# Kernel optimization log

Measured on AMD Instinct MI355X. Metric: run time of the kernel, lower is better.

## Reference

```python
import jax, jax.numpy as jnp
import numpy as np

B, S, D = 4, 1024, 1024
H, Dh = 16, 64
SPLATS_PER_LEVEL = [16, 32, 64]
LEVEL_W = [0.5, 0.3, 0.2]
TOPK = 64


def setup_inputs() -> dict:
    key = jax.random.key(0)
    ks = jax.random.split(key, 13)
    P = sum(SPLATS_PER_LEVEL)
    s = D ** -0.5
    inp = {
        'hidden_states': jax.random.normal(ks[0], (B, S, D), jnp.float32),
        'attention_mask': jnp.ones((B, S), jnp.float32),
        'Wq': jax.random.normal(ks[1], (D, H * Dh), jnp.float32) * s,
        'bq': jnp.zeros((H * Dh,), jnp.float32),
        'Wk': jax.random.normal(ks[2], (D, H * Dh), jnp.float32) * s,
        'bk': jnp.zeros((H * Dh,), jnp.float32),
        'Wv': jax.random.normal(ks[3], (D, H * Dh), jnp.float32) * s,
        'bv': jnp.zeros((H * Dh,), jnp.float32),
        'Wo': jax.random.normal(ks[4], (H * Dh, D), jnp.float32) * s,
        'bo': jnp.zeros((D,), jnp.float32),
    }
    # splat parameters in head_dim space (positions, full-covariance precisions, weights)
    mu = jax.random.normal(ks[5], (P, Dh), jnp.float32) * 0.5
    A0 = jax.random.normal(ks[6], (P, Dh, Dh), jnp.float32) * 0.1
    # SPD precision ~ inv(0.1*I) = 10*I plus small random SPD perturbation
    prec = jnp.einsum('pij,pkj->pik', A0, A0) + 10.0 * jnp.eye(Dh, dtype=jnp.float32)
    amp = jnp.abs(jax.random.normal(ks[7], (P,), jnp.float32)) + 0.5
    lw = jnp.concatenate([jnp.full((n,), w, jnp.float32) for n, w in zip(SPLATS_PER_LEVEL, LEVEL_W)])
    inp['mu'] = mu
    inp['prec'] = prec
    inp['splat_w'] = amp * lw  # amplitude * level_weight, combined
    return inp


def _split_heads(x):
    # [B,S,H*Dh] -> [B,H,S,Dh]
    return x.reshape(B, S, H, Dh).transpose(0, 2, 1, 3)


def reference(hidden_states, attention_mask, Wq, bq, Wk, bk, Wv, bv, Wo, bo, mu, prec, splat_w):
    q = _split_heads(hidden_states @ Wq + bq) * (Dh ** -0.5)
    k = _split_heads(hidden_states @ Wk + bk)  # projected but unused, as in the original
    v = _split_heads(hidden_states @ Wv + bv)

    # Gaussian splat density per token: phi_s(t) = exp(-0.5 (t-mu_s)^T P_s (t-mu_s))
    def splat_phi(mu_s, P_s):
        d = q - mu_s  # [B,H,S,Dh]
        m = jnp.einsum('bhsd,de,bhse->bhs', d, P_s, d)
        return jnp.exp(-0.5 * m)

    phi = jax.vmap(splat_phi)(mu, prec)  # [P,B,H,S]

    # hierarchical splat affinity: A[b,h,i,j] = sum_s w_s phi_s(q_i) phi_s(q_j)
    attn = jnp.einsum('pbhs,p,pbht->bhst', phi, splat_w, phi)  # [B,H,S,S]

    # top-k sparsification per row (keep top sparse_topk entries)
    thr = jax.lax.top_k(attn, TOPK)[0][..., -1:]
    attn = jnp.where(attn >= thr, attn, 0.0)

    # mask multiplies columns: extended mask[b,0,i,j] = attention_mask[b,j]
    attn = attn * attention_mask[:, None, None, :]

    # row normalization with 1e-12 floor
    row = jnp.maximum(attn.sum(axis=-1, keepdims=True), 1e-12)
    attn = attn / row

    ctx = jnp.einsum('bhst,bhtd->bhsd', attn, v)  # [B,H,S,Dh]
    ctx = ctx.transpose(0, 2, 1, 3).reshape(B, S, H * Dh)
    return ctx @ Wo + bo  # dropout is identity in eval
```

## Files before the change

### kernel.cpp

```cpp
#include <hip/hip_runtime.h>
#include <cstdint>
#include <cstddef>

#define NB 4
#define NS 1024
#define ND 1024
#define NH 16
#define NDH 64
#define NP 112
#define NTOPK 64
#define NZCAP 128
#define PCH 14

typedef _Float16 f16x8 __attribute__((ext_vector_type(8)));
typedef short bf16x8 __attribute__((ext_vector_type(8)));
typedef float f32x4 __attribute__((ext_vector_type(4)));
typedef unsigned short u16x8 __attribute__((ext_vector_type(8)));

__device__ __forceinline__ unsigned short bf16r(float f) {
  const unsigned u = __float_as_uint(f);
  return (unsigned short)((u + 0x7FFFu + ((u >> 16) & 1u)) >> 16);
}

__global__ __launch_bounds__(256) void prep_kernel(
    const float* __restrict__ mu, const float* __restrict__ prec,
    const float* __restrict__ spw, _Float16* __restrict__ Rh,
    _Float16* __restrict__ Rl, float* __restrict__ tneg,
    float* __restrict__ lswg) {
  __shared__ double A2[64][64];
  const int p = blockIdx.x;
  const int t = threadIdx.x & 63, q = threadIdx.x >> 6;

  for (int e = q; e < 64; e += 4)
    A2[e][t] = (double)prec[((size_t)p * 64 + e) * 64 + t];
  __syncthreads();

  for (int k = 0; k < 64; ++k) {
    if (threadIdx.x == k) A2[k][k] = sqrt(A2[k][k]);
    __syncthreads();
    if (q == 0 && t > k) A2[k][t] /= A2[k][k];
    __syncthreads();
    const double lik = A2[k][t];
    for (int j = k + 1 + q; j <= t; j += 4)
      A2[j][t] -= lik * A2[k][j];
    __syncthreads();
  }

  for (int d = q; d < 64; d += 4) {
    const float rv = (t >= d) ? (float)A2[d][t] : 0.f;
    const _Float16 h = (_Float16)rv;
    Rh[((size_t)p << 12) + (d << 6) + t] = h;
    Rl[((size_t)p << 12) + (d << 6) + t] =
        (_Float16)((rv - (float)h) * 2048.0f);
  }

  if (q == 0) {
    double s = 0.0;
    for (int e = t; e < 64; ++e) s += A2[t][e] * (double)mu[p * 64 + e];
    tneg[p * 64 + t] = (float)(-s);
  }
  if (threadIdx.x == 0) lswg[p] = 0.5f * logf(spw[p]);
}

__global__ __launch_bounds__(256) void split_x(
    const float* __restrict__ X, _Float16* __restrict__ Xh,
    _Float16* __restrict__ Xl) {
  const size_t i = ((size_t)blockIdx.x * 256 + threadIdx.x) * 8;
  const float4 a = *(const float4*)(X + i);
  const float4 b = *(const float4*)(X + i + 4);
  const float v[8] = {a.x, a.y, a.z, a.w, b.x, b.y, b.z, b.w};
  f16x8 hv, lv;
#pragma unroll
  for (int j = 0; j < 8; ++j) {
    const _Float16 h = (_Float16)v[j];
    hv[j] = h;
    lv[j] = (_Float16)((v[j] - (float)h) * 2048.0f);
  }
  *(f16x8*)(Xh + i) = hv;
  *(f16x8*)(Xl + i) = lv;
}

__global__ __launch_bounds__(256) void transpose_split(
    const float* __restrict__ W, _Float16* __restrict__ Th,
    _Float16* __restrict__ Tl) {
  __shared__ float T[64][65];
  const int tid = threadIdx.x;
  const int k0 = blockIdx.x * 64, n0 = blockIdx.y * 64;
  const int c = tid & 63, rb = tid >> 6;
#pragma unroll 4
  for (int i = 0; i < 16; ++i) {
    const int r = rb * 16 + i;
    T[r][c] = W[(size_t)(k0 + r) * 1024 + n0 + c];
  }
  __syncthreads();
#pragma unroll 4
  for (int i = 0; i < 16; ++i) {
    const int r = rb * 16 + i;
    const float v = T[c][r];
    const _Float16 h = (_Float16)v;
    Th[(size_t)(n0 + r) * 1024 + k0 + c] = h;
    Tl[(size_t)(n0 + r) * 1024 + k0 + c] = (_Float16)((v - (float)h) * 2048.0f);
  }
}

__global__ __launch_bounds__(256) void transpose_h(
    const float* __restrict__ W, _Float16* __restrict__ Th) {
  __shared__ float T[64][65];
  const int tid = threadIdx.x;
  const int k0 = blockIdx.x * 64, n0 = blockIdx.y * 64;
  const int c = tid & 63, rb = tid >> 6;
#pragma unroll 4
  for (int i = 0; i < 16; ++i) {
    const int r = rb * 16 + i;
    T[r][c] = W[(size_t)(k0 + r) * 1024 + n0 + c];
  }
  __syncthreads();
#pragma unroll 4
  for (int i = 0; i < 16; ++i) {
    const int r = rb * 16 + i;
    Th[(size_t)(n0 + r) * 1024 + k0 + c] = (_Float16)T[c][r];
  }
}

__global__ __launch_bounds__(256, 2) void gemmq_mfma(
    const _Float16* __restrict__ Xh, const _Float16* __restrict__ Xl,
    const _Float16* __restrict__ Wth, const _Float16* __restrict__ Wtl,
    const float* __restrict__ bias, _Float16* __restrict__ QhO,
    _Float16* __restrict__ QlO) {
  const int tid = threadIdx.x, lane = tid & 63, wv = tid >> 6;
  const int l15 = lane & 15, lhi = lane >> 4;
  const int n0 = blockIdx.x * 64;
  const int m0 = blockIdx.y * 128 + wv * 32;

  f32x4 aM[2][4], aC[2][4];
#pragma unroll
  for (int i = 0; i < 2; ++i)
#pragma unroll
    for (int j = 0; j < 4; ++j) {
      const f32x4 z = {0.f, 0.f, 0.f, 0.f};
      aM[i][j] = z; aC[i][j] = z;
    }

  const _Float16* xh0 = Xh + (size_t)(m0 + l15) * 1024 + lhi * 8;
  const _Float16* xl0 = Xl + (size_t)(m0 + l15) * 1024 + lhi * 8;
  const _Float16* wh0 = Wth + (size_t)(n0 + l15) * 1024 + lhi * 8;
  const _Float16* wl0 = Wtl + (size_t)(n0 + l15) * 1024 + lhi * 8;

#pragma unroll 4
  for (int k0 = 0; k0 < 1024; k0 += 32) {
    f16x8 ah[2], al[2], bh[4], bl[4];
#pragma unroll
    for (int mA = 0; mA < 2; ++mA) {
      ah[mA] = *(const f16x8*)(xh0 + mA * 16384 + k0);
      al[mA] = *(const f16x8*)(xl0 + mA * 16384 + k0);
    }
#pragma unroll
    for (int nB = 0; nB < 4; ++nB) {
      bh[nB] = *(const f16x8*)(wh0 + nB * 16384 + k0);
      bl[nB] = *(const f16x8*)(wl0 + nB * 16384 + k0);
    }
#pragma unroll
    for (int mA = 0; mA < 2; ++mA)
#pragma unroll
      for (int nB = 0; nB < 4; ++nB) {
        aM[mA][nB] = __builtin_amdgcn_mfma_f32_16x16x32_f16(ah[mA], bh[nB], aM[mA][nB], 0, 0, 0);
        aC[mA][nB] = __builtin_amdgcn_mfma_f32_16x16x32_f16(ah[mA], bl[nB], aC[mA][nB], 0, 0, 0);
        aC[mA][nB] = __builtin_amdgcn_mfma_f32_16x16x32_f16(al[mA], bh[nB], aC[mA][nB], 0, 0, 0);
      }
  }

  const float eps = 4.8828125e-4f;
  const int h = n0 >> 6;
  float bq[4];
#pragma unroll
  for (int nB = 0; nB < 4; ++nB) bq[nB] = bias[n0 + nB * 16 + l15];
#pragma unroll
  for (int mA = 0; mA < 2; ++mA)
#pragma unroll
    for (int nB = 0; nB < 4; ++nB) {
      const int dd = nB * 16 + l15;
#pragma unroll
      for (int r = 0; r < 4; ++r) {
        const int m = m0 + mA * 16 + lhi * 4 + r;
        const int b = m >> 10, s = m & 1023;
        const float v = (aM[mA][nB][r] + aC[mA][nB][r] * eps + bq[nB]) * 0.125f;
        const _Float16 hh = (_Float16)v;
        const size_t o = ((((size_t)b * NH + h) << 10) + s) * 64 + dd;
        QhO[o] = hh;
        QlO[o] = (_Float16)((v - (float)hh) * 2048.0f);
      }
    }
}

__global__ __launch_bounds__(256, 2) void gemmv_mfma(
    const float* __restrict__ X, const _Float16* __restrict__ Wth,
    const float* __restrict__ bias, float* __restrict__ dst,
    int moff, int bh0) {
  const int tid = threadIdx.x, lane = tid & 63, wv = tid >> 6;
  const int l15 = lane & 15, lhi = lane >> 4;
  const int n0 = blockIdx.x * 64;
  const int m0 = moff + blockIdx.y * 128 + wv * 32;

  f32x4 acc[2][4];
#pragma unroll
  for (int i = 0; i < 2; ++i)
#pragma unroll
    for (int j = 0; j < 4; ++j) {
      const f32x4 z = {0.f, 0.f, 0.f, 0.f};
      acc[i][j] = z;
    }

  const float* x0 = X + (size_t)(m0 + l15) * 1024 + lhi * 8;
  const _Float16* w0 = Wth + (size_t)(n0 + l15) * 1024 + lhi * 8;

#pragma unroll 4
  for (int k0 = 0; k0 < 1024; k0 += 32) {
    f16x8 ah[2], bh[4];
#pragma unroll
    for (int mA = 0; mA < 2; ++mA) {
      const float4 a = *(const float4*)(x0 + mA * 16384 + k0);
      const float4 b = *(const float4*)(x0 + mA * 16384 + k0 + 4);
      f16x8 hv;
      hv[0] = (_Float16)a.x; hv[1] = (_Float16)a.y;
      hv[2] = (_Float16)a.z; hv[3] = (_Float16)a.w;
      hv[4] = (_Float16)b.x; hv[5] = (_Float16)b.y;
      hv[6] = (_Float16)b.z; hv[7] = (_Float16)b.w;
      ah[mA] = hv;
    }
#pragma unroll
    for (int nB = 0; nB < 4; ++nB)
      bh[nB] = *(const f16x8*)(w0 + nB * 16384 + k0);
#pragma unroll
    for (int mA = 0; mA < 2; ++mA)
#pragma unroll
      for (int nB = 0; nB < 4; ++nB)
        acc[mA][nB] = __builtin_amdgcn_mfma_f32_16x16x32_f16(
            ah[mA], bh[nB], acc[mA][nB], 0, 0, 0);
  }

  const int h = n0 >> 6;
  float bb[4];
#pragma unroll
  for (int nB = 0; nB < 4; ++nB) bb[nB] = bias[n0 + nB * 16 + l15];
#pragma unroll
  for (int mA = 0; mA < 2; ++mA)
#pragma unroll
    for (int nB = 0; nB < 4; ++nB) {
      const int dd = nB * 16 + l15;
#pragma unroll
      for (int r = 0; r < 4; ++r) {
        const int m = m0 + mA * 16 + lhi * 4 + r;
        const int bidx = m >> 10, s = m & 1023;
        const int lbh = (bidx << 4) + h - bh0;
        dst[((((size_t)lbh << 10) + s) << 6) + dd] = acc[mA][nB][r] + bb[nB];
      }
    }
}

__global__ __launch_bounds__(256, 2) void phi3(
    const _Float16* __restrict__ Qh, const _Float16* __restrict__ Ql,
    const _Float16* __restrict__ Rh, const _Float16* __restrict__ Rl,
    const float* __restrict__ tneg, const float* __restrict__ lswg,
    float* __restrict__ Lt) {
  __shared__ __align__(16) _Float16 RhS[2][4096];
  __shared__ __align__(16) _Float16 RlS[2][4096];
  __shared__ __align__(16) float tns[PCH * 64];
  __shared__ float lsws[PCH];
  const int tid = threadIdx.x, lane = tid & 63, wv = tid >> 6;
  const int l15 = lane & 15, lhi = lane >> 4;
  const int tokbase = blockIdx.x * 256;
  const int tb = tokbase + wv * 64;
  const int pbase = blockIdx.y * PCH;
  const float eps = 4.8828125e-4f;

  for (int i = tid; i < PCH * 16; i += 256)
    ((float4*)tns)[i] = ((const float4*)(tneg + (pbase << 6)))[i];
  if (tid < PCH) lsws[tid] = lswg[pbase + tid];

  f16x8 qb[4][2][2];
#pragma unroll
  for (int T = 0; T < 4; ++T)
#pragma unroll
    for (int c = 0; c < 2; ++c) {
      const size_t off = ((size_t)(tb + T * 16 + l15) << 6) + c * 32 + lhi * 8;
      qb[T][c][0] = *(const f16x8*)(Qh + off);
      qb[T][c][1] = *(const f16x8*)(Ql + off);
    }

  f16x8 sgH[2], sgL[2];
#define PHI_LOAD(p)                                                          \
  {                                                                          \
    const _Float16* rhp = Rh + ((size_t)(pbase + (p)) << 12);                \
    const _Float16* rlp = Rl + ((size_t)(pbase + (p)) << 12);                \
    _Pragma("unroll") for (int j = 0; j < 2; ++j) {                          \
      const int X = tid * 32 + j * 16;                                       \
      const int src = X ^ (((X >> 7) & 7) << 4);                             \
      sgH[j] = *(const f16x8*)((const char*)rhp + src);                      \
      sgL[j] = *(const f16x8*)((const char*)rlp + src);                      \
    }                                                                        \
  }
#define PHI_WRITE(buf)                                                       \
  {                                                                          \
    _Pragma("unroll") for (int j = 0; j < 2; ++j) {                          \
      const int X = tid * 32 + j * 16;                                       \
      *(f16x8*)((char*)&RhS[buf][0] + X) = sgH[j];                           \
      *(f16x8*)((char*)&RlS[buf][0] + X) = sgL[j];                           \
    }                                                                        \
  }

  PHI_LOAD(0)
  PHI_WRITE(0)

  float* ub = Lt + (((size_t)(tokbase >> 10) * NP) << 10);
  const int sbase = (tb & 1023);

  for (int pi = 0; pi < PCH; ++pi) {
    __syncthreads();
    const int buf = pi & 1;
    if (pi + 1 < PCH) PHI_LOAD(pi + 1)

    float sq0 = 0.f, sq1 = 0.f, sq2 = 0.f, sq3 = 0.f;
#pragma unroll
    for (int mt = 0; mt < 4; ++mt) {
      const float4 tv = *(const float4*)&tns[(pi << 6) + mt * 16 + lhi * 4];
      const f32x4 ti = {tv.x, tv.y, tv.z, tv.w};
      const f32x4 z = {0.f, 0.f, 0.f, 0.f};
      f32x4 aM[4], aC[4];
#pragma unroll
      for (int T = 0; T < 4; ++T) { aM[T] = ti; aC[T] = z; }
#pragma unroll
      for (int c = 0; c < 2; ++c) {
        if (mt >= 2 && c == 0) continue;
        const int row = mt * 16 + l15;
        int bo = row * 128 + c * 64 + lhi * 16;
        bo ^= ((row & 7) << 4);
        const f16x8 ah = *(const f16x8*)((const char*)&RhS[buf][0] + bo);
        const f16x8 al = *(const f16x8*)((const char*)&RlS[buf][0] + bo);
#pragma unroll
        for (int T = 0; T < 4; ++T) {
          aM[T] = __builtin_amdgcn_mfma_f32_16x16x32_f16(ah, qb[T][c][0], aM[T], 0, 0, 0);
          aC[T] = __builtin_amdgcn_mfma_f32_16x16x32_f16(ah, qb[T][c][1], aC[T], 0, 0, 0);
          aC[T] = __builtin_amdgcn_mfma_f32_16x16x32_f16(al, qb[T][c][0], aC[T], 0, 0, 0);
        }
      }
#pragma unroll
      for (int r = 0; r < 4; ++r) {
        float y;
        y = aM[0][r] + aC[0][r] * eps; sq0 += y * y;
        y = aM[1][r] + aC[1][r] * eps; sq1 += y * y;
        y = aM[2][r] + aC[2][r] * eps; sq2 += y * y;
        y = aM[3][r] + aC[3][r] * eps; sq3 += y * y;
      }
    }
    sq0 += __shfl_xor(sq0, 16, 64); sq0 += __shfl_xor(sq0, 32, 64);
    sq1 += __shfl_xor(sq1, 16, 64); sq1 += __shfl_xor(sq1, 32, 64);
    sq2 += __shfl_xor(sq2, 16, 64); sq2 += __shfl_xor(sq2, 32, 64);
    sq3 += __shfl_xor(sq3, 16, 64); sq3 += __shfl_xor(sq3, 32, 64);
    const float sqs = (lhi == 0) ? sq0 : (lhi == 1) ? sq1 : (lhi == 2) ? sq2 : sq3;
    ub[((size_t)(pbase + pi) << 10) + sbase + lane] = lsws[pi] - 0.5f * sqs;

    __syncthreads();
    if (pi + 1 < PCH) PHI_WRITE(buf ^ 1)
  }
#undef PHI_LOAD
#undef PHI_WRITE
}

__global__ __launch_bounds__(256) void psi_kernel(
    const float* __restrict__ Lt, unsigned short* __restrict__ P0,
    unsigned short* __restrict__ P1, float* __restrict__ af, int bh0) {
  __shared__ unsigned short Ls[2][64 * 120];
  __shared__ float pmax[4][64];
  const int tid = threadIdx.x;
  const int lbh = blockIdx.x >> 4;
  const int gbh = bh0 + lbh;
  const int s0 = (blockIdx.x & 15) << 6;
  const int tok = tid & 63, pg = tid >> 6;

  const float* col = Lt + ((size_t)gbh * NP + pg * 28) * 1024 + s0 + tok;
  float ls[28];
  float a = -3.4e38f;
#pragma unroll
  for (int j = 0; j < 28; ++j) {
    ls[j] = col[(size_t)j << 10];
    a = fmaxf(a, ls[j]);
  }
  pmax[pg][tok] = a;
  __syncthreads();
  a = fmaxf(fmaxf(pmax[0][tok], pmax[1][tok]),
            fmaxf(pmax[2][tok], pmax[3][tok]));
  if (pg == 0) af[(gbh << 10) + s0 + tok] = a;

  const int rbase = tok * 120 + pg * 28;
#pragma unroll
  for (int jj = 0; jj < 14; ++jj) {
    unsigned short v0[2], v1[2];
#pragma unroll
    for (int e = 0; e < 2; ++e) {
      const float x = expf(ls[jj * 2 + e] - a);
      const unsigned short b0 = bf16r(x);
      const float f0 = __uint_as_float((unsigned)b0 << 16);
      const unsigned short b1 = bf16r((x - f0) * 256.0f);
      if (e == 0) { v0[0] = b0; v0[1] = b1; }
      else        { v1[0] = b0; v1[1] = b1; }
    }
#pragma unroll
    for (int pl = 0; pl < 2; ++pl) {
      ushort2 pk; pk.x = v0[pl]; pk.y = v1[pl];
      *(ushort2*)&Ls[pl][rbase + jj * 2] = pk;
    }
  }
  __syncthreads();

  const size_t gb = (size_t)((lbh << 10) + s0) * NP;
#pragma unroll 1
  for (int pl = 0; pl < 2; ++pl) {
    unsigned short* dst = (pl == 0 ? P0 : P1) + gb;
    const unsigned short* src = &Ls[pl][0];
    for (int i = tid; i < 896; i += 256) {
      const int t2 = i / 14;
      const int off = (i - t2 * 14) * 8;
      *(u16x8*)(dst + t2 * 112 + off) = *(const u16x8*)(src + t2 * 120 + off);
    }
  }
}

#define GADDR(row, col) \
  (((row) << 11) + ((((col) << 1) ^ ((((row) >> 2) & 3) << 5))))

__global__ __launch_bounds__(512) void attn7_kernel(
    const unsigned short* __restrict__ P0, const unsigned short* __restrict__ P1,
    const float* __restrict__ af, const float* __restrict__ V,
    const float* __restrict__ amask, _Float16* __restrict__ ctxh, int bh0) {
  __shared__ __align__(16) _Float16 Ath[32 * 1024];
  __shared__ __align__(16) float eajs[1024];
  __shared__ __align__(16) float msks[1024];
  const int tid = threadIdx.x;
  const int id = blockIdx.x;
  const int bhl = ((id >> 8) << 3) | (id & 7);
  const int gbh = bh0 + bhl;
  const int i0 = ((id >> 3) & 31) * 32;
  const int bidx = gbh >> 4;
  const int h = gbh & 15;
  const int lane = tid & 63, wv = tid >> 6;
  const int l15 = lane & 15, lhi = lane >> 4;
  const float* afb = af + (gbh << 10);
  char* Ab = (char*)Ath;

  eajs[tid] = expf(afb[tid]);
  eajs[tid + 512] = expf(afb[tid + 512]);
  msks[tid] = amask[(bidx << 10) + tid];
  msks[tid + 512] = amask[(bidx << 10) + tid + 512];

  {
    const unsigned short* Pb0 = P0 + (size_t)(bhl << 10) * NP;
    const unsigned short* Pb1 = P1 + (size_t)(bhl << 10) * NP;
    const bf16x8 zz = {0, 0, 0, 0, 0, 0, 0, 0};
    const int rt = wv >> 2;
    const int jw = wv & 3;
    bf16x8 A0[4], A1[4];
    {
      const size_t ro = (size_t)(i0 + rt * 16 + l15) * NP;
#pragma unroll
      for (int c = 0; c < 3; ++c) {
        A0[c] = *(const bf16x8*)(Pb0 + ro + c * 32 + lhi * 8);
        A1[c] = *(const bf16x8*)(Pb1 + ro + c * 32 + lhi * 8);
      }
      A0[3] = (lhi < 2) ? *(const bf16x8*)(Pb0 + ro + 96 + lhi * 8) : zz;
      A1[3] = (lhi < 2) ? *(const bf16x8*)(Pb1 + ro + 96 + lhi * 8) : zz;
    }

#define LOADB(dst, Pb, jtv)                                                  \
  {                                                                          \
    const size_t co = (size_t)((jtv) * 16 + l15) * NP;                       \
    _Pragma("unroll") for (int c = 0; c < 3; ++c)                            \
        dst[c] = *(const bf16x8*)(Pb + co + c * 32 + lhi * 8);               \
    dst[3] = (lhi < 2) ? *(const bf16x8*)(Pb + co + 96 + lhi * 8) : zz;      \
  }

    bf16x8 B0c[4], B1c[4], B0n[4];
    LOADB(B0c, Pb0, jw * 16)
    LOADB(B1c, Pb1, jw * 16)

#pragma unroll 1
    for (int jt16 = 0; jt16 < 16; ++jt16) {
      const int jt = jw * 16 + jt16;
      if (jt16 < 15) LOADB(B0n, Pb0, jt + 1)
      f32x4 g0 = {0.f, 0.f, 0.f, 0.f};
      f32x4 g1a = {0.f, 0.f, 0.f, 0.f}, g1b = {0.f, 0.f, 0.f, 0.f};
      __builtin_amdgcn_s_setprio(1);
#pragma unroll
      for (int c = 0; c < 4; ++c) {
        g0  = __builtin_amdgcn_mfma_f32_16x16x32_bf16(A0[c], B0c[c], g0, 0, 0, 0);
        g1a = __builtin_amdgcn_mfma_f32_16x16x32_bf16(A0[c], B1c[c], g1a, 0, 0, 0);
        g1b = __builtin_amdgcn_mfma_f32_16x16x32_bf16(A1[c], B0c[c], g1b, 0, 0, 0);
      }
      __builtin_amdgcn_s_setprio(0);
#pragma unroll
      for (int r = 0; r < 4; ++r) {
        const float g = fmaxf(g0[r] + (g1a[r] + g1b[r]) * 0.00390625f, 0.f);
        *(_Float16*)(Ab + GADDR(rt * 16 + lhi * 4 + r, jt * 16 + l15)) =
            (_Float16)g;
      }
      if (jt16 < 15) {
        LOADB(B1c, Pb1, jt + 1)
#pragma unroll
        for (int c = 0; c < 4; ++c) B0c[c] = B0n[c];
      }
    }
#undef LOADB
  }
  __syncthreads();

  {
    const float* Vb = V + ((size_t)bhl << 16);
    int cnts[4];

#pragma unroll
    for (int rr = 0; rr < 4; ++rr) {
      const int r = wv * 4 + rr;
      const float eai = expf(afb[i0 + r]);
      float fv[16], fm[16];
      float mx = 0.f;
#pragma unroll
      for (int k = 0; k < 16; ++k) {
        const int j = k * 64 + lane;
        const float gv = (float)*(const _Float16*)(Ab + GADDR(r, j));
        fv[k] = eai * (eajs[j] * gv);
        fm[k] = fv[k] * msks[j];
        mx = fmaxf(mx, fv[k]);
      }
#pragma unroll
      for (int off = 32; off > 0; off >>= 1) mx = fmaxf(mx, __shfl_xor(mx, off, 64));
      const unsigned mu = __float_as_uint(mx);
      const int startbit = (mu == 0u) ? 0 : (31 - __clz(mu));
      unsigned c = 0u;
      for (int bit = startbit; bit >= 0; --bit) {
        const unsigned cand = c | (1u << bit);
        int cnt = 0;
#pragma unroll
        for (int k = 0; k < 16; ++k)
          cnt += (int)__popcll(__ballot(__float_as_uint(fv[k]) >= cand));
        if (cnt >= NTOPK) {
          c = cand;
          if (cnt == NTOPK) break;
        }
      }
      const float thr = __uint_as_float(c);
      float ssum = 0.f;
#pragma unroll
      for (int k = 0; k < 16; ++k) ssum += (fv[k] >= thr) ? fm[k] : 0.f;
#pragma unroll
      for (int off = 32; off > 0; off >>= 1) ssum += __shfl_xor(ssum, off, 64);
      const float inv = 1.0f / fmaxf(ssum, 1e-12f);

      float* nzv = (float*)(Ab + (r << 11));
      int* nzi = (int*)(Ab + (r << 11) + 512);
      unsigned cnt = 0;
#pragma unroll
      for (int k = 0; k < 16; ++k) {
        const bool keep = (fv[k] >= thr) && (fm[k] > 0.f);
        const unsigned long long b = __ballot(keep);
        if (keep) {
          const unsigned pos = cnt + (unsigned)__popcll(b & ((1ull << lane) - 1ull));
          if (pos < NZCAP) {
            nzi[pos] = k * 64 + lane;
            nzv[pos] = fm[k] * inv;
          }
        }
        cnt += (unsigned)__popcll(b);
      }
      cnts[rr] = (int)(cnt < NZCAP ? cnt : NZCAP);
    }

#pragma unroll
    for (int rr = 0; rr < 4; ++rr) {
      const int r = wv * 4 + rr;
      const float* nzv = (const float*)(Ab + (r << 11));
      const int* nzi = (const int*)(Ab + (r << 11) + 512);
      const int n = cnts[rr];
      float a0 = 0.f, a1 = 0.f, a2 = 0.f, a3 = 0.f;
      int t = 0;
      for (; t + 8 <= n; t += 8) {
        const int j0 = nzi[t], j1 = nzi[t + 1], j2 = nzi[t + 2], j3 = nzi[t + 3];
        const int j4 = nzi[t + 4], j5 = nzi[t + 5], j6 = nzi[t + 6], j7 = nzi[t + 7];
        const float w0 = nzv[t], w1 = nzv[t + 1], w2 = nzv[t + 2], w3 = nzv[t + 3];
        const float w4 = nzv[t + 4], w5 = nzv[t + 5], w6 = nzv[t + 6], w7 = nzv[t + 7];
        const float v0 = Vb[(j0 << 6) + lane];
        const float v1 = Vb[(j1 << 6) + lane];
        const float v2 = Vb[(j2 << 6) + lane];
        const float v3 = Vb[(j3 << 6) + lane];
        const float v4 = Vb[(j4 << 6) + lane];
        const float v5 = Vb[(j5 << 6) + lane];
        const float v6 = Vb[(j6 << 6) + lane];
        const float v7 = Vb[(j7 << 6) + lane];
        a0 += w0 * v0; a1 += w1 * v1; a2 += w2 * v2; a3 += w3 * v3;
        a0 += w4 * v4; a1 += w5 * v5; a2 += w6 * v6; a3 += w7 * v7;
      }
      for (; t < n; ++t) a0 += nzv[t] * Vb[(nzi[t] << 6) + lane];
      const float s = ((a0 + a1) + (a2 + a3)) * 0x1p80f;
      ctxh[(size_t)((bidx << 10) + i0 + r) * 1024 + (h << 6) + lane] =
          (_Float16)s;
    }
  }
}

__global__ __launch_bounds__(256, 2) void gemmo_mfma(
    const _Float16* __restrict__ Ch, const _Float16* __restrict__ Wth,
    const _Float16* __restrict__ Wtl, const float* __restrict__ bias,
    float* __restrict__ out) {
  const int tid = threadIdx.x, lane = tid & 63, wv = tid >> 6;
  const int l15 = lane & 15, lhi = lane >> 4;
  const int n0 = blockIdx.x * 64;
  const int m0 = blockIdx.y * 128 + wv * 32;

  f32x4 aM[2][4], aC[2][4];
#pragma unroll
  for (int i = 0; i < 2; ++i)
#pragma unroll
    for (int j = 0; j < 4; ++j) {
      const f32x4 z = {0.f, 0.f, 0.f, 0.f};
      aM[i][j] = z; aC[i][j] = z;
    }

  const _Float16* xh0 = Ch + (size_t)(m0 + l15) * 1024 + lhi * 8;
  const _Float16* wh0 = Wth + (size_t)(n0 + l15) * 1024 + lhi * 8;
  const _Float16* wl0 = Wtl + (size_t)(n0 + l15) * 1024 + lhi * 8;

#pragma unroll 4
  for (int k0 = 0; k0 < 1024; k0 += 32) {
    f16x8 ah[2], bh[4], bl[4];
#pragma unroll
    for (int mA = 0; mA < 2; ++mA)
      ah[mA] = *(const f16x8*)(xh0 + mA * 16384 + k0);
#pragma unroll
    for (int nB = 0; nB < 4; ++nB) {
      bh[nB] = *(const f16x8*)(wh0 + nB * 16384 + k0);
      bl[nB] = *(const f16x8*)(wl0 + nB * 16384 + k0);
    }
#pragma unroll
    for (int mA = 0; mA < 2; ++mA)
#pragma unroll
      for (int nB = 0; nB < 4; ++nB) {
        aM[mA][nB] = __builtin_amdgcn_mfma_f32_16x16x32_f16(ah[mA], bh[nB], aM[mA][nB], 0, 0, 0);
        aC[mA][nB] = __builtin_amdgcn_mfma_f32_16x16x32_f16(ah[mA], bl[nB], aC[mA][nB], 0, 0, 0);
      }
  }

  const float eps = 4.8828125e-4f;
  const float unscale = 0x1p-80f;
  float bb[4];
#pragma unroll
  for (int nB = 0; nB < 4; ++nB) bb[nB] = bias[n0 + nB * 16 + l15];
#pragma unroll
  for (int mA = 0; mA < 2; ++mA)
#pragma unroll
    for (int nB = 0; nB < 4; ++nB) {
      const int n = n0 + nB * 16 + l15;
#pragma unroll
      for (int r = 0; r < 4; ++r) {
        const int m = m0 + mA * 16 + lhi * 4 + r;
        out[(size_t)m * 1024 + n] =
            (aM[mA][nB][r] + aC[mA][nB][r] * eps) * unscale + bb[nB];
      }
    }
}

extern "C" void kernel_launch(void* const* d_in, const int* in_sizes, int n_in,
                              void* d_out, int out_size, void* d_ws,
                              size_t ws_size, hipStream_t stream) {
  (void)in_sizes; (void)n_in; (void)out_size; (void)ws_size;
  const float* hs    = (const float*)d_in[0];
  const float* amask = (const float*)d_in[1];
  const float* Wq    = (const float*)d_in[2];
  const float* bq    = (const float*)d_in[3];
  const float* Wv    = (const float*)d_in[6];
  const float* bv    = (const float*)d_in[7];
  const float* Wo    = (const float*)d_in[8];
  const float* bo    = (const float*)d_in[9];
  const float* mu    = (const float*)d_in[10];
  const float* prec  = (const float*)d_in[11];
  const float* spw   = (const float*)d_in[12];
  float* out = (float*)d_out;

  float* w = (float*)d_ws;
  _Float16* Xh   = (_Float16*)w;
  _Float16* Xl   = (_Float16*)(w + 2097152);
  _Float16* Rh   = (_Float16*)w;
  _Float16* Rl   = (_Float16*)(w + 229376);
  float*    tneg = w + 458752;
  float*    lswg = w + 465920;
  unsigned short* P0 = (unsigned short*)w;
  unsigned short* P1 = (unsigned short*)(w + 1835008);
  _Float16* Qh   = (_Float16*)(w + 4194304);
  _Float16* Ql   = (_Float16*)(w + 6291456);
  float*    V    = w + 5505024;
  float*    af   = w + 7602176;
  _Float16* Wvth = (_Float16*)(w + 7667712);
  _Float16* Wqth = (_Float16*)(w + 8388608);
  _Float16* Wqtl = (_Float16*)(w + 8912896);
  float*    Lt   = w + 8388608;
  _Float16* ctxh = (_Float16*)(w + 8388608);
  _Float16* Woth = (_Float16*)w;
  _Float16* Wotl = (_Float16*)(w + 524288);

  split_x<<<dim3(2048), dim3(256), 0, stream>>>(hs, Xh, Xl);
  transpose_split<<<dim3(16, 16), dim3(256), 0, stream>>>(Wq, Wqth, Wqtl);
  gemmq_mfma<<<dim3(16, 32), dim3(256), 0, stream>>>(Xh, Xl, Wqth, Wqtl, bq, Qh, Ql);
  prep_kernel<<<dim3(NP), dim3(256), 0, stream>>>(mu, prec, spw, Rh, Rl, tneg, lswg);
  phi3<<<dim3(256, 8), dim3(256), 0, stream>>>(Qh, Ql, Rh, Rl, tneg, lswg, Lt);
  transpose_h<<<dim3(16, 16), dim3(256), 0, stream>>>(Wv, Wvth);
  for (int half = 0; half < 2; ++half) {
    const int bh0 = half * 32;
    psi_kernel<<<dim3(512), dim3(256), 0, stream>>>(Lt, P0, P1, af, bh0);
    gemmv_mfma<<<dim3(16, 16), dim3(256), 0, stream>>>(hs, Wvth, bv, V,
                                                       half * 2048, bh0);
    attn7_kernel<<<dim3(1024), dim3(512), 0, stream>>>(P0, P1, af, V, amask,
                                                       ctxh, bh0);
  }
  transpose_split<<<dim3(16, 16), dim3(256), 0, stream>>>(Wo, Woth, Wotl);
  gemmo_mfma<<<dim3(16, 32), dim3(256), 0, stream>>>(ctxh, Woth, Wotl, bo, out);
}
```

Baseline: 648.7 us.

## Merge two-half psi/gemmv/attn launches into single full-size launches with new workspace layout

```diff
diff --git a/kernel.cpp b/kernel.cpp
--- a/kernel.cpp
+++ b/kernel.cpp
@@ -194,12 +194,11 @@
 
 __global__ __launch_bounds__(256, 2) void gemmv_mfma(
     const float* __restrict__ X, const _Float16* __restrict__ Wth,
-    const float* __restrict__ bias, float* __restrict__ dst,
-    int moff, int bh0) {
+    const float* __restrict__ bias, float* __restrict__ dst) {
   const int tid = threadIdx.x, lane = tid & 63, wv = tid >> 6;
   const int l15 = lane & 15, lhi = lane >> 4;
   const int n0 = blockIdx.x * 64;
-  const int m0 = moff + blockIdx.y * 128 + wv * 32;
+  const int m0 = blockIdx.y * 128 + wv * 32;
 
   f32x4 acc[2][4];
 #pragma unroll
@@ -251,8 +250,8 @@
       for (int r = 0; r < 4; ++r) {
         const int m = m0 + mA * 16 + lhi * 4 + r;
         const int bidx = m >> 10, s = m & 1023;
-        const int lbh = (bidx << 4) + h - bh0;
-        dst[((((size_t)lbh << 10) + s) << 6) + dd] = acc[mA][nB][r] + bb[nB];
+        const int bh_ = (bidx << 4) + h;
+        dst[((((size_t)bh_ << 10) + s) << 6) + dd] = acc[mA][nB][r] + bb[nB];
       }
     }
 }
@@ -368,12 +367,11 @@
 
 __global__ __launch_bounds__(256) void psi_kernel(
     const float* __restrict__ Lt, unsigned short* __restrict__ P0,
-    unsigned short* __restrict__ P1, float* __restrict__ af, int bh0) {
+    unsigned short* __restrict__ P1, float* __restrict__ af) {
   __shared__ unsigned short Ls[2][64 * 120];
   __shared__ float pmax[4][64];
   const int tid = threadIdx.x;
-  const int lbh = blockIdx.x >> 4;
-  const int gbh = bh0 + lbh;
+  const int gbh = blockIdx.x >> 4;
   const int s0 = (blockIdx.x & 15) << 6;
   const int tok = tid & 63, pg = tid >> 6;
 
@@ -412,7 +410,7 @@
   }
   __syncthreads();
 
-  const size_t gb = (size_t)((lbh << 10) + s0) * NP;
+  const size_t gb = (size_t)((gbh << 10) + s0) * NP;
 #pragma unroll 1
   for (int pl = 0; pl < 2; ++pl) {
     unsigned short* dst = (pl == 0 ? P0 : P1) + gb;
@@ -428,17 +426,16 @@
 #define GADDR(row, col) \
   (((row) << 11) + ((((col) << 1) ^ ((((row) >> 2) & 3) << 5))))
 
-__global__ __launch_bounds__(512) void attn7_kernel(
+__global__ __launch_bounds__(512) void attn8_kernel(
     const unsigned short* __restrict__ P0, const unsigned short* __restrict__ P1,
     const float* __restrict__ af, const float* __restrict__ V,
-    const float* __restrict__ amask, _Float16* __restrict__ ctxh, int bh0) {
+    const float* __restrict__ amask, _Float16* __restrict__ ctxh) {
   __shared__ __align__(16) _Float16 Ath[32 * 1024];
   __shared__ __align__(16) float eajs[1024];
   __shared__ __align__(16) float msks[1024];
   const int tid = threadIdx.x;
   const int id = blockIdx.x;
-  const int bhl = ((id >> 8) << 3) | (id & 7);
-  const int gbh = bh0 + bhl;
+  const int gbh = ((id >> 8) << 3) | (id & 7);
   const int i0 = ((id >> 3) & 31) * 32;
   const int bidx = gbh >> 4;
   const int h = gbh & 15;
@@ -453,8 +450,8 @@
   msks[tid + 512] = amask[(bidx << 10) + tid + 512];
 
   {
-    const unsigned short* Pb0 = P0 + (size_t)(bhl << 10) * NP;
-    const unsigned short* Pb1 = P1 + (size_t)(bhl << 10) * NP;
+    const unsigned short* Pb0 = P0 + (size_t)(gbh << 10) * NP;
+    const unsigned short* Pb1 = P1 + (size_t)(gbh << 10) * NP;
     const bf16x8 zz = {0, 0, 0, 0, 0, 0, 0, 0};
     const int rt = wv >> 2;
     const int jw = wv & 3;
@@ -513,7 +510,7 @@
   __syncthreads();
 
   {
-    const float* Vb = V + ((size_t)bhl << 16);
+    const float* Vb = V + ((size_t)gbh << 16);
     int cnts[4];
 
 #pragma unroll
@@ -581,21 +578,33 @@
       const int n = cnts[rr];
       float a0 = 0.f, a1 = 0.f, a2 = 0.f, a3 = 0.f;
       int t = 0;
+      for (; t + 16 <= n; t += 16) {
+        int jj[16]; float ww[16], vv[16];
+#pragma unroll
+        for (int u = 0; u < 16; ++u) { jj[u] = nzi[t + u]; ww[u] = nzv[t + u]; }
+#pragma unroll
+        for (int u = 0; u < 16; ++u) vv[u] = Vb[(jj[u] << 6) + lane];
+#pragma unroll
+        for (int u = 0; u < 16; ++u) {
+          if ((u & 3) == 0) a0 += ww[u] * vv[u];
+          else if ((u & 3) == 1) a1 += ww[u] * vv[u];
+          else if ((u & 3) == 2) a2 += ww[u] * vv[u];
+          else a3 += ww[u] * vv[u];
+        }
+      }
       for (; t + 8 <= n; t += 8) {
-        const int j0 = nzi[t], j1 = nzi[t + 1], j2 = nzi[t + 2], j3 = nzi[t + 3];
-        const int j4 = nzi[t + 4], j5 = nzi[t + 5], j6 = nzi[t + 6], j7 = nzi[t + 7];
-        const float w0 = nzv[t], w1 = nzv[t + 1], w2 = nzv[t + 2], w3 = nzv[t + 3];
-        const float w4 = nzv[t + 4], w5 = nzv[t + 5], w6 = nzv[t + 6], w7 = nzv[t + 7];
-        const float v0 = Vb[(j0 << 6) + lane];
-        const float v1 = Vb[(j1 << 6) + lane];
-        const float v2 = Vb[(j2 << 6) + lane];
-        const float v3 = Vb[(j3 << 6) + lane];
-        const float v4 = Vb[(j4 << 6) + lane];
-        const float v5 = Vb[(j5 << 6) + lane];
-        const float v6 = Vb[(j6 << 6) + lane];
-        const float v7 = Vb[(j7 << 6) + lane];
-        a0 += w0 * v0; a1 += w1 * v1; a2 += w2 * v2; a3 += w3 * v3;
-        a0 += w4 * v4; a1 += w5 * v5; a2 += w6 * v6; a3 += w7 * v7;
+        int jj[8]; float ww[8], vv[8];
+#pragma unroll
+        for (int u = 0; u < 8; ++u) { jj[u] = nzi[t + u]; ww[u] = nzv[t + u]; }
+#pragma unroll
+        for (int u = 0; u < 8; ++u) vv[u] = Vb[(jj[u] << 6) + lane];
+#pragma unroll
+        for (int u = 0; u < 8; ++u) {
+          if ((u & 3) == 0) a0 += ww[u] * vv[u];
+          else if ((u & 3) == 1) a1 += ww[u] * vv[u];
+          else if ((u & 3) == 2) a2 += ww[u] * vv[u];
+          else a3 += ww[u] * vv[u];
+        }
       }
       for (; t < n; ++t) a0 += nzv[t] * Vb[(nzi[t] << 6) + lane];
       const float s = ((a0 + a1) + (a2 + a3)) * 0x1p80f;
@@ -691,16 +700,16 @@
   float*    tneg = w + 458752;
   float*    lswg = w + 465920;
   unsigned short* P0 = (unsigned short*)w;
-  unsigned short* P1 = (unsigned short*)(w + 1835008);
+  unsigned short* P1 = (unsigned short*)(w + 3670016);
   _Float16* Qh   = (_Float16*)(w + 4194304);
   _Float16* Ql   = (_Float16*)(w + 6291456);
-  float*    V    = w + 5505024;
-  float*    af   = w + 7602176;
-  _Float16* Wvth = (_Float16*)(w + 7667712);
+  float*    af   = w + 7340032;
+  _Float16* Wvth = (_Float16*)(w + 7405568);
   _Float16* Wqth = (_Float16*)(w + 8388608);
   _Float16* Wqtl = (_Float16*)(w + 8912896);
   float*    Lt   = w + 8388608;
-  _Float16* ctxh = (_Float16*)(w + 8388608);
+  float*    V    = w + 8388608;
+  _Float16* ctxh = (_Float16*)(w + 12582912);
   _Float16* Woth = (_Float16*)w;
   _Float16* Wotl = (_Float16*)(w + 524288);
 
@@ -709,15 +718,10 @@
   gemmq_mfma<<<dim3(16, 32), dim3(256), 0, stream>>>(Xh, Xl, Wqth, Wqtl, bq, Qh, Ql);
   prep_kernel<<<dim3(NP), dim3(256), 0, stream>>>(mu, prec, spw, Rh, Rl, tneg, lswg);
   phi3<<<dim3(256, 8), dim3(256), 0, stream>>>(Qh, Ql, Rh, Rl, tneg, lswg, Lt);
+  psi_kernel<<<dim3(1024), dim3(256), 0, stream>>>(Lt, P0, P1, af);
   transpose_h<<<dim3(16, 16), dim3(256), 0, stream>>>(Wv, Wvth);
-  for (int half = 0; half < 2; ++half) {
-    const int bh0 = half * 32;
-    psi_kernel<<<dim3(512), dim3(256), 0, stream>>>(Lt, P0, P1, af, bh0);
-    gemmv_mfma<<<dim3(16, 16), dim3(256), 0, stream>>>(hs, Wvth, bv, V,
-                                                       half * 2048, bh0);
-    attn7_kernel<<<dim3(1024), dim3(512), 0, stream>>>(P0, P1, af, V, amask,
-                                                       ctxh, bh0);
-  }
+  gemmv_mfma<<<dim3(16, 32), dim3(256), 0, stream>>>(hs, Wvth, bv, V);
+  attn8_kernel<<<dim3(2048), dim3(512), 0, stream>>>(P0, P1, af, V, amask, ctxh);
   transpose_split<<<dim3(16, 16), dim3(256), 0, stream>>>(Wo, Woth, Wotl);
   gemmo_mfma<<<dim3(16, 32), dim3(256), 0, stream>>>(ctxh, Woth, Wotl, bo, out);
 }
```

Result: faster. 594.8 us (-8.3%).
